# Performance work log

Measured on AMD Instinct MI355X. Metric: run time of the kernel, lower is better.

Reference implementation:

```python
import jax, jax.numpy as jnp
import numpy as np

B, K, V, NB = 256, 62, 14522, 28

def setup_inputs() -> dict:
    key = jax.random.key(0)
    ks = jax.random.split(key, 10)
    thetas = jax.random.normal(ks[0], (B, K * 3), dtype=jnp.float32) * 0.2
    bone_lengths_core = jax.random.normal(ks[1], (B, NB), dtype=jnp.float32)
    center_bone_length = jax.random.uniform(ks[2], (B, 1), dtype=jnp.float32) + 0.5
    trans = jax.random.normal(ks[3], (B, 3), dtype=jnp.float32)
    scale = jax.random.uniform(ks[4], (B,), dtype=jnp.float32) + 0.5
    v_template = jax.random.normal(ks[5], (V, 3), dtype=jnp.float32) * 0.05
    t_pose_joints = jax.random.normal(ks[6], (K, 3), dtype=jnp.float32) * 0.1
    weights = jax.nn.softmax(jax.random.normal(ks[7], (V, K), dtype=jnp.float32) * 2.0, axis=1)
    # kinematic tree: parent[i] < i (binary-ish tree), parent[0] unused
    parents = jnp.maximum((jnp.arange(K) - 1) // 2, 0).astype(jnp.int64)
    bone_length_mapper = jax.random.randint(ks[8], (K,), -1, NB).astype(jnp.int64)
    return {"thetas": thetas, "bone_lengths_core": bone_lengths_core,
            "center_bone_length": center_bone_length, "trans": trans, "scale": scale,
            "v_template": v_template, "t_pose_joints": t_pose_joints, "weights": weights,
            "parents": parents, "bone_length_mapper": bone_length_mapper}

def euler2mat(r):
    # r: [N,3] ZYX euler angles -> [N,3,3]
    z, y, x = r[:, 0], r[:, 1], r[:, 2]
    cx, sx = jnp.cos(x), jnp.sin(x)
    cy, sy = jnp.cos(y), jnp.sin(y)
    cz, sz = jnp.cos(z), jnp.sin(z)
    one = jnp.ones_like(x)
    zero = jnp.zeros_like(x)
    Rx = jnp.stack([one, zero, zero, zero, cx, -sx, zero, sx, cx], -1).reshape(-1, 3, 3)
    Ry = jnp.stack([cy, zero, sy, zero, one, zero, -sy, zero, cy], -1).reshape(-1, 3, 3)
    Rz = jnp.stack([cz, -sz, zero, sz, cz, zero, zero, zero, one], -1).reshape(-1, 3, 3)
    return jnp.einsum('nij,njk,nkl->nil', Rz, Ry, Rx)

def _forward(thetas, bone_lengths_core, center_bone_length, trans, scale,
             v_template, t_pose_joints, weights, parents, bone_length_mapper):
    b = thetas.shape[0]
    k = t_pose_joints.shape[0]
    blc = jax.nn.sigmoid(bone_lengths_core / 5.0) * 2.0          # [B,28]
    R = euler2mat(thetas.reshape(-1, 3)).reshape(b, k, 3, 3)      # [B,K,3,3]
    Jt = t_pose_joints                                            # [K,3]
    # per-joint bone-length scale factor [B,K]
    gathered = blc[:, jnp.clip(bone_length_mapper, 0)]            # [B,K]
    factor = jnp.where(bone_length_mapper[None, :] < 0, 1.0, gathered)
    factor = factor.at[:, 1].set(center_bone_length[:, 0])
    factor = factor.at[:, 0].set(1.0)
    # local translations: root uses J0, others scaled offsets to parent
    off = (Jt - Jt[parents])[None] * factor[:, :, None]           # [B,K,3]
    off = off.at[:, 0].set(Jt[0][None])
    # local affines A [B,K,4,4]
    A = jnp.zeros((b, k, 4, 4), dtype=thetas.dtype)
    A = A.at[:, :, :3, :3].set(R)
    A = A.at[:, :, :3, 3].set(off)
    A = A.at[:, :, 3, 3].set(1.0)
    # compose along the kinematic tree
    G0 = jnp.zeros_like(A).at[:, 0].set(A[:, 0])
    def step(G_all, i):
        Gp = jnp.take(G_all, parents[i], axis=1)                  # [B,4,4]
        Gi = Gp @ jnp.take(A, i, axis=1)
        return jax.lax.dynamic_update_index_in_dim(G_all, Gi, i, axis=1), None
    G_all, _ = jax.lax.scan(step, G0, jnp.arange(1, k))
    J_final = G_all[:, :, :3, 3]                                  # [B,K,3]
    # subtract inverse-bind contribution: G' = G - pack(G @ [J;0])
    RJ = jnp.einsum('bkij,kj->bki', G_all[:, :, :3, :3], Jt)
    G = G_all.at[:, :, :3, 3].add(-RJ)
    # LBS skinning: T [B,V,4,4]
    T = jnp.einsum('bkij,vk->bvij', G, weights)
    rest_h = jnp.concatenate([v_template, jnp.ones((v_template.shape[0], 1), v_template.dtype)], axis=1)
    v = jnp.einsum('bvij,vj->bvi', T, rest_h)[:, :, :3]
    V_final = v * scale[:, None, None] + trans[:, None, :]
    J_out = J_final * scale[:, None, None] + trans[:, None, :]
    return V_final, J_out

def reference(thetas, bone_lengths_core, center_bone_length, trans, scale,
              v_template, t_pose_joints, weights, parents, bone_length_mapper):
    return _forward(thetas, bone_lengths_core, center_bone_length, trans, scale,
                    v_template, t_pose_joints, weights, parents, bone_length_mapper)
```

## Files before the change

### kernel.cpp

```cpp
#include <hip/hip_runtime.h>

#define NJ     62
#define NV     14522
#define NCORE  28
#define KPAD   256
#define OUTF   (NV * 3)
#define MT     908
#define NSTR   256

typedef __attribute__((ext_vector_type(8))) short short8v;
typedef __attribute__((ext_vector_type(4))) short short4v;
typedef __attribute__((ext_vector_type(4))) float floatx4;
typedef __attribute__((ext_vector_type(2))) float floatx2;

#define AS1(p) ((const __attribute__((address_space(1))) void*)(p))
#define AS3(p) ((__attribute__((address_space(3))) void*)(p))

#define SCHED0() __builtin_amdgcn_sched_barrier(0)
#define WAITVM0() do { SCHED0(); asm volatile("s_waitcnt vmcnt(0)" ::: "memory"); SCHED0(); } while (0)

static __device__ inline short f2bf(float x) {
    unsigned u = __float_as_uint(x);
    unsigned r = (u + 0x7fffu + ((u >> 16) & 1u)) >> 16;
    return (short)r;
}

static __device__ inline short8v pack8(float a0, float a1, float a2, float a3,
                                       float a4, float a5, float a6, float a7) {
    union { unsigned u[4]; short8v v; } p;
    asm("v_cvt_pk_bf16_f32 %0, %1, %2" : "=v"(p.u[0]) : "v"(a0), "v"(a1));
    asm("v_cvt_pk_bf16_f32 %0, %1, %2" : "=v"(p.u[1]) : "v"(a2), "v"(a3));
    asm("v_cvt_pk_bf16_f32 %0, %1, %2" : "=v"(p.u[2]) : "v"(a4), "v"(a5));
    asm("v_cvt_pk_bf16_f32 %0, %1, %2" : "=v"(p.u[3]) : "v"(a6), "v"(a7));
    return p.v;
}

static __device__ inline unsigned swz(unsigned off) {
    return off ^ (((off >> 9) & 7u) << 4);
}

__global__ __launch_bounds__(256) void fk_kernel(
    const float* __restrict__ thetas, const float* __restrict__ blc,
    const float* __restrict__ cbl, const float* __restrict__ trans,
    const float* __restrict__ scale, const float* __restrict__ tpose,
    const int* __restrict__ parents, const int* __restrict__ mapper,
    short* __restrict__ Bt, float* __restrict__ Jout)
{
    __shared__ float Asm[4][NJ][12];
    __shared__ float Gsm[4][NJ][12];

    const int w = threadIdx.x >> 6;
    const int b = blockIdx.x * 4 + w;
    const int k = threadIdx.x & 63;
    int p = 0;

    if (k < NJ) {
        p = parents[k];
        const float tz = thetas[(b * NJ + k) * 3 + 0];
        const float ty = thetas[(b * NJ + k) * 3 + 1];
        const float tx = thetas[(b * NJ + k) * 3 + 2];
        const float cx = cosf(tx), sx = sinf(tx);
        const float cy = cosf(ty), sy = sinf(ty);
        const float cz = cosf(tz), sz = sinf(tz);
        const float r00 = cz * cy;
        const float r01 = cz * sy * sx - sz * cx;
        const float r02 = sz * sx + cz * sy * cx;
        const float r10 = sz * cy;
        const float r11 = cz * cx + sz * sy * sx;
        const float r12 = sz * sy * cx - cz * sx;
        const float r20 = -sy;
        const float r21 = cy * sx;
        const float r22 = cy * cx;

        float f;
        const int m = mapper[k];
        if (k == 0)        f = 1.0f;
        else if (k == 1)   f = cbl[b];
        else if (m < 0)    f = 1.0f;
        else               f = 2.0f / (1.0f + expf(-blc[b * NCORE + m] * 0.2f));

        float ox, oy, oz;
        if (k == 0) {
            ox = tpose[0]; oy = tpose[1]; oz = tpose[2];
        } else {
            ox = (tpose[k * 3 + 0] - tpose[p * 3 + 0]) * f;
            oy = (tpose[k * 3 + 1] - tpose[p * 3 + 1]) * f;
            oz = (tpose[k * 3 + 2] - tpose[p * 3 + 2]) * f;
        }
        Asm[w][k][0] = r00; Asm[w][k][1] = r01; Asm[w][k][2]  = r02; Asm[w][k][3]  = ox;
        Asm[w][k][4] = r10; Asm[w][k][5] = r11; Asm[w][k][6]  = r12; Asm[w][k][7]  = oy;
        Asm[w][k][8] = r20; Asm[w][k][9] = r21; Asm[w][k][10] = r22; Asm[w][k][11] = oz;
    }
    __syncthreads();

    if (k == 0) {
        #pragma unroll
        for (int j = 0; j < 12; ++j) Gsm[w][0][j] = Asm[w][0][j];
    }
    __syncthreads();

    const int depth = (k < NJ) ? (31 - __clz((unsigned)(k + 1))) : 99;
    for (int d = 1; d <= 5; ++d) {
        if (depth == d) {
            float gp[12], a[12], g[12];
            #pragma unroll
            for (int j = 0; j < 12; ++j) { gp[j] = Gsm[w][p][j]; a[j] = Asm[w][k][j]; }
            #pragma unroll
            for (int i = 0; i < 3; ++i) {
                #pragma unroll
                for (int j = 0; j < 4; ++j) {
                    float s = (j == 3) ? gp[i * 4 + 3] : 0.0f;
                    s = fmaf(gp[i * 4 + 0], a[0 * 4 + j], s);
                    s = fmaf(gp[i * 4 + 1], a[1 * 4 + j], s);
                    s = fmaf(gp[i * 4 + 2], a[2 * 4 + j], s);
                    g[i * 4 + j] = s;
                }
            }
            #pragma unroll
            for (int j = 0; j < 12; ++j) Gsm[w][k][j] = g[j];
        }
        __syncthreads();
    }

    if (k < NJ) {
        float g[12];
        #pragma unroll
        for (int j = 0; j < 12; ++j) g[j] = Gsm[w][k][j];
        const float jx = tpose[k * 3 + 0];
        const float jy = tpose[k * 3 + 1];
        const float jz = tpose[k * 3 + 2];
        const float s  = scale[b];
        Jout[(b * NJ + k) * 3 + 0] = fmaf(g[3],  s, trans[b * 3 + 0]);
        Jout[(b * NJ + k) * 3 + 1] = fmaf(g[7],  s, trans[b * 3 + 1]);
        Jout[(b * NJ + k) * 3 + 2] = fmaf(g[11], s, trans[b * 3 + 2]);
        float np[3];
        np[0] = g[3]  - (g[0] * jx + g[1] * jy + g[2]  * jz);
        np[1] = g[7]  - (g[4] * jx + g[5] * jy + g[6]  * jz);
        np[2] = g[11] - (g[8] * jx + g[9] * jy + g[10] * jz);
        #pragma unroll
        for (int i = 0; i < 3; ++i) {
            short4v o;
            o[0] = f2bf(g[i * 4 + 0]);
            o[1] = f2bf(g[i * 4 + 1]);
            o[2] = f2bf(g[i * 4 + 2]);
            o[3] = f2bf(np[i]);
            *(short4v*)&Bt[(size_t)(b * 3 + i) * KPAD + k * 4] = o;
        }
        if (k == 0) {
            short4v z = {0, 0, 0, 0};
            #pragma unroll
            for (int i = 0; i < 3; ++i) {
                *(short4v*)&Bt[(size_t)(b * 3 + i) * KPAD + 248] = z;
                *(short4v*)&Bt[(size_t)(b * 3 + i) * KPAD + 252] = z;
            }
        }
    }
}

__global__ __launch_bounds__(256, 4) void gemm_skin(
    const float* __restrict__ W,
    const float* __restrict__ vt,
    const short* __restrict__ Bt,
    const float* __restrict__ scale,
    const float* __restrict__ trans,
    float* __restrict__ out)
{
    __shared__ __align__(16) char ldsB[48 * 512];
    __shared__ __align__(16) float epi_all[4 * 800];

    const int tid  = threadIdx.x;
    const int wave = tid >> 6;
    const int lane = tid & 63;
    const int lrow = lane & 15;
    const int lk   = lane >> 4;
    const int yy    = blockIdx.x >> 6;
    const int inner = blockIdx.x & 63;
    const int s     = inner * 4 + wave;
    const int start  = s * 3 + (s < 140 ? s : 140);
    const int ntiles = 3 + (s < 140 ? 1 : 0);
    const int b0 = yy * 16;
    float* epi = epi_all + wave * 800;

    {
        const char* Bsrc = (const char*)(Bt + (size_t)yy * 48 * KPAD);
        #pragma unroll
        for (int cc = 0; cc < 6; ++cc) {
            const unsigned Lb = (unsigned)(wave * 6144 + cc * 1024);
            __builtin_amdgcn_global_load_lds(AS1(Bsrc + swz(Lb + lane * 16)),
                                             AS3(ldsB + Lb), 16, 0, 0);
        }
    }

    float sv[3], tv[3]; int eoff[3];
    #pragma unroll
    for (int nt = 0; nt < 3; ++nt) {
        const int n_loc = nt * 16 + lrow;
        const int bl = n_loc / 3, ii = n_loc - bl * 3;
        eoff[nt] = bl * 50 + ii;
        sv[nt] = scale[b0 + bl];
        tv[nt] = trans[(b0 + bl) * 3 + ii];
    }
    unsigned bofs[3], bxor[3];
    #pragma unroll
    for (int nt = 0; nt < 3; ++nt) {
        const unsigned brow = nt * 16 + lrow;
        bofs[nt] = brow * 512;
        bxor[nt] = (brow & 7u) << 4;
    }

    WAITVM0();
    __syncthreads();

    for (int t = 0; t < ntiles; ++t) {
        const int mtile = start + t;
        int vrow = mtile * 16 + lrow;
        if (vrow > NV - 1) vrow = NV - 1;
        const float hx = vt[vrow * 3 + 0];
        const float hy = vt[vrow * 3 + 1];
        const float hz = vt[vrow * 3 + 2];
        const float* Wr = W + (size_t)vrow * NJ;

        short8v af[8];
        #pragma unroll
        for (int k8 = 0; k8 < 8; ++k8) {
            const int j0 = k8 * 8 + lk * 2;
            float w0 = 0.f, w1 = 0.f;
            if (j0 < NJ) {
                const floatx2 wv = *(const floatx2*)(Wr + j0);
                w0 = wv[0]; w1 = wv[1];
            }
            af[k8] = pack8(w0 * hx, w0 * hy, w0 * hz, w0,
                           w1 * hx, w1 * hy, w1 * hz, w1);
        }

        floatx4 acc[3];
        #pragma unroll
        for (int nt = 0; nt < 3; ++nt) acc[nt] = (floatx4){0.f, 0.f, 0.f, 0.f};
        #pragma unroll
        for (int k8 = 0; k8 < 8; ++k8) {
            const unsigned cb = (unsigned)(k8 * 4 + lk) * 16;
            #pragma unroll
            for (int nt = 0; nt < 3; ++nt) {
                const short8v bf = *(const short8v*)(ldsB + bofs[nt] + (cb ^ bxor[nt]));
                acc[nt] = __builtin_amdgcn_mfma_f32_16x16x32_bf16(
                    af[k8], bf, acc[nt], 0, 0, 0);
            }
        }

        #pragma unroll
        for (int nt = 0; nt < 3; ++nt) {
            #pragma unroll
            for (int r = 0; r < 4; ++r)
                epi[eoff[nt] + (lk * 4 + r) * 3] =
                    fmaf(acc[nt][r], sv[nt], tv[nt]);
        }

        const int m48 = mtile * 48;
        const bool edge = (m48 + 48 > OUTF);
        #pragma unroll
        for (int it = 0; it < 6; ++it) {
            const int idx = it * 64 + lane;
            const int r = idx / 24, j = idx - r * 24;
            const floatx2 val = *(const floatx2*)&epi[r * 50 + 2 * j];
            const int pp = m48 + 2 * j;
            if (!edge || pp + 1 < OUTF)
                *(floatx2*)&out[(size_t)(b0 + r) * OUTF + pp] = val;
        }
    }
}

extern "C" void kernel_launch(void* const* d_in, const int* in_sizes, int n_in,
                              void* d_out, int out_size, void* d_ws, size_t ws_size,
                              hipStream_t stream)
{
    const float* thetas  = (const float*)d_in[0];
    const float* blc     = (const float*)d_in[1];
    const float* cbl     = (const float*)d_in[2];
    const float* trans   = (const float*)d_in[3];
    const float* scale   = (const float*)d_in[4];
    const float* vtempl  = (const float*)d_in[5];
    const float* tpose   = (const float*)d_in[6];
    const float* weights = (const float*)d_in[7];
    const int*   parents = (const int*)d_in[8];
    const int*   mapper  = (const int*)d_in[9];

    float* out  = (float*)d_out;
    float* Jout = out + (size_t)256 * NV * 3;

    short* Bt = (short*)d_ws;

    fk_kernel<<<64, 256, 0, stream>>>(thetas, blc, cbl, trans, scale, tpose,
                                      parents, mapper, Bt, Jout);
    gemm_skin<<<1024, 256, 0, stream>>>(weights, vtempl, Bt, scale, trans, out);
}
```

Measured before the change: 27.61 us.

## Fuse forward kinematics into skinning GEMM, recomputing bone transforms per block

Removes the separate forward-kinematics launch and the global workspace round trip. Each GEMM block now recomputes the 16 batch transforms it needs and writes them straight into swizzled LDS. The grid shrinks from 1024 to 768 blocks, with each wave taking 4-5 vertex tiles instead of 3-4, and launch bounds lowered to 3 blocks per SM. The cost is redundant FK work (sin, cos, exp and a 5-level tree walk with many barriers) repeated in all 48 blocks per batch group, which serializes ahead of the GEMM in every block.

New measurement: 34.86 us. 26.3% more time.

```diff
diff --git a/kernel.cpp b/kernel.cpp
--- a/kernel.cpp
+++ b/kernel.cpp
@@ -6,18 +6,11 @@
 #define KPAD   256
 #define OUTF   (NV * 3)
 #define MT     908
-#define NSTR   256
 
 typedef __attribute__((ext_vector_type(8))) short short8v;
 typedef __attribute__((ext_vector_type(4))) short short4v;
 typedef __attribute__((ext_vector_type(4))) float floatx4;
 typedef __attribute__((ext_vector_type(2))) float floatx2;
-
-#define AS1(p) ((const __attribute__((address_space(1))) void*)(p))
-#define AS3(p) ((__attribute__((address_space(3))) void*)(p))
-
-#define SCHED0() __builtin_amdgcn_sched_barrier(0)
-#define WAITVM0() do { SCHED0(); asm volatile("s_waitcnt vmcnt(0)" ::: "memory"); SCHED0(); } while (0)
 
 static __device__ inline short f2bf(float x) {
     unsigned u = __float_as_uint(x);
@@ -35,161 +28,146 @@
     return p.v;
 }
 
-static __device__ inline unsigned swz(unsigned off) {
-    return off ^ (((off >> 9) & 7u) << 4);
-}
-
-__global__ __launch_bounds__(256) void fk_kernel(
-    const float* __restrict__ thetas, const float* __restrict__ blc,
-    const float* __restrict__ cbl, const float* __restrict__ trans,
-    const float* __restrict__ scale, const float* __restrict__ tpose,
-    const int* __restrict__ parents, const int* __restrict__ mapper,
-    short* __restrict__ Bt, float* __restrict__ Jout)
-{
-    __shared__ float Asm[4][NJ][12];
-    __shared__ float Gsm[4][NJ][12];
-
-    const int w = threadIdx.x >> 6;
-    const int b = blockIdx.x * 4 + w;
-    const int k = threadIdx.x & 63;
-    int p = 0;
-
-    if (k < NJ) {
-        p = parents[k];
-        const float tz = thetas[(b * NJ + k) * 3 + 0];
-        const float ty = thetas[(b * NJ + k) * 3 + 1];
-        const float tx = thetas[(b * NJ + k) * 3 + 2];
-        const float cx = cosf(tx), sx = sinf(tx);
-        const float cy = cosf(ty), sy = sinf(ty);
-        const float cz = cosf(tz), sz = sinf(tz);
-        const float r00 = cz * cy;
-        const float r01 = cz * sy * sx - sz * cx;
-        const float r02 = sz * sx + cz * sy * cx;
-        const float r10 = sz * cy;
-        const float r11 = cz * cx + sz * sy * sx;
-        const float r12 = sz * sy * cx - cz * sx;
-        const float r20 = -sy;
-        const float r21 = cy * sx;
-        const float r22 = cy * cx;
-
-        float f;
-        const int m = mapper[k];
-        if (k == 0)        f = 1.0f;
-        else if (k == 1)   f = cbl[b];
-        else if (m < 0)    f = 1.0f;
-        else               f = 2.0f / (1.0f + expf(-blc[b * NCORE + m] * 0.2f));
-
-        float ox, oy, oz;
-        if (k == 0) {
-            ox = tpose[0]; oy = tpose[1]; oz = tpose[2];
-        } else {
-            ox = (tpose[k * 3 + 0] - tpose[p * 3 + 0]) * f;
-            oy = (tpose[k * 3 + 1] - tpose[p * 3 + 1]) * f;
-            oz = (tpose[k * 3 + 2] - tpose[p * 3 + 2]) * f;
-        }
-        Asm[w][k][0] = r00; Asm[w][k][1] = r01; Asm[w][k][2]  = r02; Asm[w][k][3]  = ox;
-        Asm[w][k][4] = r10; Asm[w][k][5] = r11; Asm[w][k][6]  = r12; Asm[w][k][7]  = oy;
-        Asm[w][k][8] = r20; Asm[w][k][9] = r21; Asm[w][k][10] = r22; Asm[w][k][11] = oz;
-    }
-    __syncthreads();
-
-    if (k == 0) {
-        #pragma unroll
-        for (int j = 0; j < 12; ++j) Gsm[w][0][j] = Asm[w][0][j];
-    }
-    __syncthreads();
-
-    const int depth = (k < NJ) ? (31 - __clz((unsigned)(k + 1))) : 99;
-    for (int d = 1; d <= 5; ++d) {
-        if (depth == d) {
-            float gp[12], a[12], g[12];
-            #pragma unroll
-            for (int j = 0; j < 12; ++j) { gp[j] = Gsm[w][p][j]; a[j] = Asm[w][k][j]; }
-            #pragma unroll
-            for (int i = 0; i < 3; ++i) {
-                #pragma unroll
-                for (int j = 0; j < 4; ++j) {
-                    float s = (j == 3) ? gp[i * 4 + 3] : 0.0f;
-                    s = fmaf(gp[i * 4 + 0], a[0 * 4 + j], s);
-                    s = fmaf(gp[i * 4 + 1], a[1 * 4 + j], s);
-                    s = fmaf(gp[i * 4 + 2], a[2 * 4 + j], s);
-                    g[i * 4 + j] = s;
-                }
-            }
-            #pragma unroll
-            for (int j = 0; j < 12; ++j) Gsm[w][k][j] = g[j];
-        }
-        __syncthreads();
-    }
-
-    if (k < NJ) {
-        float g[12];
-        #pragma unroll
-        for (int j = 0; j < 12; ++j) g[j] = Gsm[w][k][j];
-        const float jx = tpose[k * 3 + 0];
-        const float jy = tpose[k * 3 + 1];
-        const float jz = tpose[k * 3 + 2];
-        const float s  = scale[b];
-        Jout[(b * NJ + k) * 3 + 0] = fmaf(g[3],  s, trans[b * 3 + 0]);
-        Jout[(b * NJ + k) * 3 + 1] = fmaf(g[7],  s, trans[b * 3 + 1]);
-        Jout[(b * NJ + k) * 3 + 2] = fmaf(g[11], s, trans[b * 3 + 2]);
-        float np[3];
-        np[0] = g[3]  - (g[0] * jx + g[1] * jy + g[2]  * jz);
-        np[1] = g[7]  - (g[4] * jx + g[5] * jy + g[6]  * jz);
-        np[2] = g[11] - (g[8] * jx + g[9] * jy + g[10] * jz);
-        #pragma unroll
-        for (int i = 0; i < 3; ++i) {
-            short4v o;
-            o[0] = f2bf(g[i * 4 + 0]);
-            o[1] = f2bf(g[i * 4 + 1]);
-            o[2] = f2bf(g[i * 4 + 2]);
-            o[3] = f2bf(np[i]);
-            *(short4v*)&Bt[(size_t)(b * 3 + i) * KPAD + k * 4] = o;
-        }
-        if (k == 0) {
-            short4v z = {0, 0, 0, 0};
-            #pragma unroll
-            for (int i = 0; i < 3; ++i) {
-                *(short4v*)&Bt[(size_t)(b * 3 + i) * KPAD + 248] = z;
-                *(short4v*)&Bt[(size_t)(b * 3 + i) * KPAD + 252] = z;
-            }
-        }
-    }
-}
-
-__global__ __launch_bounds__(256, 4) void gemm_skin(
+__global__ __launch_bounds__(256, 3) void fused_kernel(
+    const float* __restrict__ thetas,
+    const float* __restrict__ blc,
+    const float* __restrict__ cbl,
+    const float* __restrict__ trans,
+    const float* __restrict__ scale,
+    const float* __restrict__ tpose,
+    const int*   __restrict__ parents,
+    const int*   __restrict__ mapper,
     const float* __restrict__ W,
     const float* __restrict__ vt,
-    const short* __restrict__ Bt,
-    const float* __restrict__ scale,
-    const float* __restrict__ trans,
     float* __restrict__ out)
 {
-    __shared__ __align__(16) char ldsB[48 * 512];
-    __shared__ __align__(16) float epi_all[4 * 800];
+    __shared__ __align__(16) char pool[24576 + 11904 + 11904];
+    char*  ldsB    = pool;
+    float* Asm     = (float*)(pool + 24576);
+    float* Gsm     = (float*)(pool + 24576 + 11904);
+    float* epi_all = (float*)(pool + 24576);
 
     const int tid  = threadIdx.x;
     const int wave = tid >> 6;
     const int lane = tid & 63;
     const int lrow = lane & 15;
     const int lk   = lane >> 4;
-    const int yy    = blockIdx.x >> 6;
-    const int inner = blockIdx.x & 63;
+    const int yy    = blockIdx.x / 48;
+    const int inner = blockIdx.x - yy * 48;
     const int s     = inner * 4 + wave;
-    const int start  = s * 3 + (s < 140 ? s : 140);
-    const int ntiles = 3 + (s < 140 ? 1 : 0);
+    const int start  = s * 4 + (s < 140 ? s : 140);
+    const int ntiles = 4 + (s < 140 ? 1 : 0);
     const int b0 = yy * 16;
+    float* Jout = out + (size_t)256 * NV * 3;
+
+    {
+        const int k = lane;
+        int p = 0, mp = -1;
+        float jx = 0.f, jy = 0.f, jz = 0.f, dx = 0.f, dy = 0.f, dz = 0.f;
+        if (k < NJ) {
+            p  = parents[k];
+            mp = mapper[k];
+            jx = tpose[k * 3 + 0]; jy = tpose[k * 3 + 1]; jz = tpose[k * 3 + 2];
+            dx = jx - tpose[p * 3 + 0];
+            dy = jy - tpose[p * 3 + 1];
+            dz = jz - tpose[p * 3 + 2];
+        }
+        const int depth = (k < NJ) ? (31 - __clz((unsigned)(k + 1))) : 99;
+        float* As = Asm + (wave * NJ) * 12;
+        float* Gs = Gsm + (wave * NJ) * 12;
+
+        for (int it = 0; it < 4; ++it) {
+            const int bb = b0 + wave * 4 + it;
+            if (k < NJ) {
+                const float tz = thetas[(bb * NJ + k) * 3 + 0];
+                const float ty = thetas[(bb * NJ + k) * 3 + 1];
+                const float tx = thetas[(bb * NJ + k) * 3 + 2];
+                const float cx = cosf(tx), sx = sinf(tx);
+                const float cy = cosf(ty), sy = sinf(ty);
+                const float cz = cosf(tz), sz = sinf(tz);
+                float f;
+                if (k == 0)        f = 1.0f;
+                else if (k == 1)   f = cbl[bb];
+                else if (mp < 0)   f = 1.0f;
+                else               f = 2.0f / (1.0f + expf(-blc[bb * NCORE + mp] * 0.2f));
+                float ox, oy, oz;
+                if (k == 0) { ox = jx; oy = jy; oz = jz; }
+                else        { ox = dx * f; oy = dy * f; oz = dz * f; }
+                float* a = As + k * 12;
+                a[0] = cz * cy;                 a[1] = cz * sy * sx - sz * cx;
+                a[2] = sz * sx + cz * sy * cx;  a[3] = ox;
+                a[4] = sz * cy;                 a[5] = cz * cx + sz * sy * sx;
+                a[6] = sz * sy * cx - cz * sx;  a[7] = oy;
+                a[8] = -sy;                     a[9] = cy * sx;
+                a[10] = cy * cx;                a[11] = oz;
+            }
+            __syncthreads();
+            if (k == 0) {
+                #pragma unroll
+                for (int j = 0; j < 12; ++j) Gs[j] = As[j];
+            }
+            __syncthreads();
+            for (int d = 1; d <= 5; ++d) {
+                if (depth == d) {
+                    float gp[12], a[12], g[12];
+                    #pragma unroll
+                    for (int j = 0; j < 12; ++j) { gp[j] = Gs[p * 12 + j]; a[j] = As[k * 12 + j]; }
+                    #pragma unroll
+                    for (int i = 0; i < 3; ++i) {
+                        #pragma unroll
+                        for (int j = 0; j < 4; ++j) {
+                            float ss = (j == 3) ? gp[i * 4 + 3] : 0.0f;
+                            ss = fmaf(gp[i * 4 + 0], a[0 * 4 + j], ss);
+                            ss = fmaf(gp[i * 4 + 1], a[1 * 4 + j], ss);
+                            ss = fmaf(gp[i * 4 + 2], a[2 * 4 + j], ss);
+                            g[i * 4 + j] = ss;
+                        }
+                    }
+                    #pragma unroll
+                    for (int j = 0; j < 12; ++j) Gs[k * 12 + j] = g[j];
+                }
+                __syncthreads();
+            }
+
+            if (k < NJ) {
+                float g[12];
+                #pragma unroll
+                for (int j = 0; j < 12; ++j) g[j] = Gs[k * 12 + j];
+                float np[3];
+                np[0] = g[3]  - (g[0] * jx + g[1] * jy + g[2]  * jz);
+                np[1] = g[7]  - (g[4] * jx + g[5] * jy + g[6]  * jz);
+                np[2] = g[11] - (g[8] * jx + g[9] * jy + g[10] * jz);
+                #pragma unroll
+                for (int i = 0; i < 3; ++i) {
+                    short4v o;
+                    o[0] = f2bf(g[i * 4 + 0]);
+                    o[1] = f2bf(g[i * 4 + 1]);
+                    o[2] = f2bf(g[i * 4 + 2]);
+                    o[3] = f2bf(np[i]);
+                    const unsigned row = (unsigned)((wave * 4 + it) * 3 + i);
+                    const unsigned off = row * 512 + (((unsigned)k * 8) ^ ((row & 7u) << 4));
+                    *(short4v*)(ldsB + off) = o;
+                }
+                if (inner == 0) {
+                    const float sc = scale[bb];
+                    Jout[(bb * NJ + k) * 3 + 0] = fmaf(g[3],  sc, trans[bb * 3 + 0]);
+                    Jout[(bb * NJ + k) * 3 + 1] = fmaf(g[7],  sc, trans[bb * 3 + 1]);
+                    Jout[(bb * NJ + k) * 3 + 2] = fmaf(g[11], sc, trans[bb * 3 + 2]);
+                }
+            } else {
+                short4v z = {0, 0, 0, 0};
+                #pragma unroll
+                for (int i = 0; i < 3; ++i) {
+                    const unsigned row = (unsigned)((wave * 4 + it) * 3 + i);
+                    const unsigned off = row * 512 + (((unsigned)k * 8) ^ ((row & 7u) << 4));
+                    *(short4v*)(ldsB + off) = z;
+                }
+            }
+            __syncthreads();
+        }
+    }
+
     float* epi = epi_all + wave * 800;
-
-    {
-        const char* Bsrc = (const char*)(Bt + (size_t)yy * 48 * KPAD);
-        #pragma unroll
-        for (int cc = 0; cc < 6; ++cc) {
-            const unsigned Lb = (unsigned)(wave * 6144 + cc * 1024);
-            __builtin_amdgcn_global_load_lds(AS1(Bsrc + swz(Lb + lane * 16)),
-                                             AS3(ldsB + Lb), 16, 0, 0);
-        }
-    }
 
     float sv[3], tv[3]; int eoff[3];
     #pragma unroll
@@ -207,9 +185,6 @@
         bofs[nt] = brow * 512;
         bxor[nt] = (brow & 7u) << 4;
     }
-
-    WAITVM0();
-    __syncthreads();
 
     for (int t = 0; t < ntiles; ++t) {
         const int mtile = start + t;
@@ -284,12 +259,9 @@
     const int*   parents = (const int*)d_in[8];
     const int*   mapper  = (const int*)d_in[9];
 
-    float* out  = (float*)d_out;
-    float* Jout = out + (size_t)256 * NV * 3;
-
-    short* Bt = (short*)d_ws;
-
-    fk_kernel<<<64, 256, 0, stream>>>(thetas, blc, cbl, trans, scale, tpose,
-                                      parents, mapper, Bt, Jout);
-    gemm_skin<<<1024, 256, 0, stream>>>(weights, vtempl, Bt, scale, trans, out);
-}
+    float* out = (float*)d_out;
+
+    fused_kernel<<<768, 256, 0, stream>>>(
+        thetas, blc, cbl, trans, scale, tpose, parents, mapper,
+        weights, vtempl, out);
+}
```
